# Optimization experiments

Hardware: AMD Instinct MI355X
Metric: run time of the kernel (lower is better)

Reference implementation:

```python
import jax, jax.numpy as jnp
import numpy as np

TOP_K = 2


def setup_inputs() -> dict:
    key = jax.random.key(0)
    k_x, k_w = jax.random.split(key)
    B, S, D, E = 4, 4096, 2048, 64
    x = jax.random.normal(k_x, (B, S, D), dtype=jnp.float32)
    # nn.Linear weight has shape [num_experts, d_model]
    W_r = jax.random.normal(k_w, (E, D), dtype=jnp.float32) * (1.0 / np.sqrt(D))
    return {"x": x, "W_r": W_r}


def reference(x, W_r):
    # router logits: [B, S, E]
    logits = jnp.einsum("bsd,ed->bse", x, W_r)
    router_probs = jax.nn.softmax(logits, axis=-1)
    gate_weights, expert_idx = jax.lax.top_k(router_probs, TOP_K)
    gate_weights = gate_weights / jnp.sum(gate_weights, axis=-1, keepdims=True)
    return gate_weights, expert_idx, router_probs
```

## Files before the change

### kernel.cpp

```cpp
#include <hip/hip_runtime.h>
#include <stdint.h>
#include <math.h>

#define D    2048
#define E    64
#define ROWS 16384
#define RG   64
#define BK   64
#define EW   16

typedef const __attribute__((address_space(1))) unsigned int guint;
typedef __attribute__((address_space(3))) unsigned int luint;
typedef __attribute__((ext_vector_type(16))) float f32x16;

__device__ __forceinline__ void gl_lds16(const float* g, float* l) {
    __builtin_amdgcn_global_load_lds((guint*)g, (luint*)l, 16, 0, 0);
}

template<int NSPLIT>
__global__ __launch_bounds__(256, 4)
void logits_kernel(const float* __restrict__ x, const float* __restrict__ Wr,
                   float* __restrict__ P) {
    __shared__ float XS[2][RG * BK];

    const int tid  = threadIdx.x;
    const int lane = tid & 63;
    const int wu   = __builtin_amdgcn_readfirstlane(tid >> 6);
    const int bid  = blockIdx.x;
    const int ks   = bid % NSPLIT;
    const int rg   = bid / NSPLIT;
    const int row0 = rg * RG;
    const int kbase = ks * (D / NSPLIT);
    const int NCH  = (D / NSPLIT) / BK;

    const float* xg[4];
#pragma unroll
    for (int i = 0; i < 4; ++i) {
        const int row = i * 16 + (tid >> 4);
        const int kq  = ((tid & 15) ^ (row & 7)) * 4;
        xg[i] = x + (size_t)(row0 + row) * D + kbase + kq;
    }
    float* const xsl0 = &XS[0][tid * 4];
    float* const xsl1 = &XS[1][tid * 4];

#define STAGE(buf, kc) do {                                                   \
        _Pragma("unroll")                                                     \
        for (int i = 0; i < 4; ++i)                                           \
            gl_lds16(xg[i] + (kc) * BK, ((buf) ? xsl1 : xsl0) + i * 1024);    \
    } while (0)

    const int eb = wu * EW;
    const float* const wbase = Wr + (size_t)eb * D + kbase;

    float acc[EW];
#pragma unroll
    for (int e = 0; e < EW; ++e) acc[e] = 0.0f;

    STAGE(0, 0);
    __syncthreads();

    const int swf = (lane & 7) * 4;
    int cur = 0;
    for (int c = 0; c < NCH; ++c) {
        if (c + 1 < NCH) STAGE(cur ^ 1, c + 1);

        float4 xv[16];
        const float* xr = &XS[cur][lane * BK];
#pragma unroll
        for (int q = 0; q < 16; ++q)
            xv[q] = *(const float4*)(xr + ((q * 4) ^ swf));

#pragma unroll
        for (int e = 0; e < EW; ++e) {
            const float* wr_ = wbase + (size_t)e * D + c * BK;
#pragma unroll
            for (int g = 0; g < 4; ++g) {
                const f32x16 wv = *(const f32x16*)(wr_ + g * 16);
#pragma unroll
                for (int j = 0; j < 4; ++j) {
                    const float4 xq = xv[g * 4 + j];
                    acc[e] = fmaf(xq.x, wv[j * 4 + 0], acc[e]);
                    acc[e] = fmaf(xq.y, wv[j * 4 + 1], acc[e]);
                    acc[e] = fmaf(xq.z, wv[j * 4 + 2], acc[e]);
                    acc[e] = fmaf(xq.w, wv[j * 4 + 3], acc[e]);
                }
            }
        }
        __syncthreads();
        cur ^= 1;
    }

    float* const pr = P + ((size_t)ks * ROWS + row0 + lane) * E + eb;
#pragma unroll
    for (int e = 0; e < EW; ++e) pr[e] = acc[e];
#undef STAGE
}

template<int NSPLIT>
__global__ __launch_bounds__(256, 8)
void finish_kernel(const float* __restrict__ P, float* __restrict__ out) {
    const int lane = threadIdx.x & 63;
    const int w    = threadIdx.x >> 6;
    const int row  = blockIdx.x * 4 + w;

    float v = 0.0f;
#pragma unroll
    for (int s = 0; s < NSPLIT; ++s)
        v += P[((size_t)s * ROWS + row) * E + lane];

    float* const out_gw    = out;
    float* const out_idx   = out + 32768;
    float* const out_probs = out + 65536;

    float m = v;
#pragma unroll
    for (int off = 32; off; off >>= 1) m = fmaxf(m, __shfl_xor(m, off));
    const float p = __expf(v - m);
    float s = p;
#pragma unroll
    for (int off = 32; off; off >>= 1) s += __shfl_xor(s, off);
    const float inv_s = 1.0f / s;

    out_probs[(size_t)row * 64 + lane] = p * inv_s;

    float v1 = v; int i1 = lane;
#pragma unroll
    for (int off = 32; off; off >>= 1) {
        const float ov = __shfl_xor(v1, off);
        const int   oi = __shfl_xor(i1, off);
        if (ov > v1 || (ov == v1 && oi < i1)) { v1 = ov; i1 = oi; }
    }
    float v2 = (lane == i1) ? -INFINITY : v; int i2 = lane;
#pragma unroll
    for (int off = 32; off; off >>= 1) {
        const float ov = __shfl_xor(v2, off);
        const int   oi = __shfl_xor(i2, off);
        if (ov > v2 || (ov == v2 && oi < i2)) { v2 = ov; i2 = oi; }
    }

    if (lane == 0) {
        const float p1 = __expf(v1 - m) * inv_s;
        const float p2 = __expf(v2 - m) * inv_s;
        const float inv12 = 1.0f / (p1 + p2);
        out_gw[(size_t)row * 2 + 0]  = p1 * inv12;
        out_gw[(size_t)row * 2 + 1]  = p2 * inv12;
        out_idx[(size_t)row * 2 + 0] = (float)i1;
        out_idx[(size_t)row * 2 + 1] = (float)i2;
    }
}

extern "C" void kernel_launch(void* const* d_in, const int* in_sizes, int n_in,
                              void* d_out, int out_size, void* d_ws, size_t ws_size,
                              hipStream_t stream) {
    const float* x  = (const float*)d_in[0];
    const float* Wr = (const float*)d_in[1];
    float* out = (float*)d_out;
    float* P   = (float*)d_ws;

    const size_t need4 = (size_t)4 * ROWS * E * sizeof(float);
    if (ws_size >= need4) {
        hipLaunchKernelGGL((logits_kernel<4>), dim3(256 * 4), dim3(256), 0, stream, x, Wr, P);
        hipLaunchKernelGGL((finish_kernel<4>), dim3(ROWS / 4), dim3(256), 0, stream, P, out);
    } else {
        hipLaunchKernelGGL((logits_kernel<1>), dim3(256), dim3(256), 0, stream, x, Wr, P);
        hipLaunchKernelGGL((finish_kernel<1>), dim3(ROWS / 4), dim3(256), 0, stream, P, out);
    }
}
```

Measured before the change: 112.1 us.

## Enlarge row tile to 256 rows per block with 4 rows per thread

Each block now covers 256 rows instead of 64, and each thread accumulates 4 rows by 16 experts, so every W_r float4 load is reused across 4 rows. This cuts repeated global and L1 reads of the router weights. The grid shrinks to 256 blocks, each using 128KB of LDS at 1 block per CU, and the barrier moves to the start of each chunk after an explicit vmcnt wait. The price is lower occupancy, more register pressure from 64 accumulators, and fewer blocks than CUs available to hide latency.

```diff
diff --git a/kernel.cpp b/kernel.cpp
--- a/kernel.cpp
+++ b/kernel.cpp
@@ -5,23 +5,22 @@
 #define D    2048
 #define E    64
 #define ROWS 16384
-#define RG   64
+#define RB   256
 #define BK   64
 #define EW   16
 
 typedef const __attribute__((address_space(1))) unsigned int guint;
 typedef __attribute__((address_space(3))) unsigned int luint;
-typedef __attribute__((ext_vector_type(16))) float f32x16;
 
 __device__ __forceinline__ void gl_lds16(const float* g, float* l) {
     __builtin_amdgcn_global_load_lds((guint*)g, (luint*)l, 16, 0, 0);
 }
 
 template<int NSPLIT>
-__global__ __launch_bounds__(256, 4)
+__global__ __launch_bounds__(256, 1)
 void logits_kernel(const float* __restrict__ x, const float* __restrict__ Wr,
                    float* __restrict__ P) {
-    __shared__ float XS[2][RG * BK];
+    __shared__ float XS[2][RB * BK];
 
     const int tid  = threadIdx.x;
     const int lane = tid & 63;
@@ -29,70 +28,78 @@
     const int bid  = blockIdx.x;
     const int ks   = bid % NSPLIT;
     const int rg   = bid / NSPLIT;
-    const int row0 = rg * RG;
-    const int kbase = ks * (D / NSPLIT);
+    const int row0 = rg * RB;
+    const int kb   = ks * (D / NSPLIT);
     const int NCH  = (D / NSPLIT) / BK;
 
-    const float* xg[4];
-#pragma unroll
-    for (int i = 0; i < 4; ++i) {
-        const int row = i * 16 + (tid >> 4);
-        const int kq  = ((tid & 15) ^ (row & 7)) * 4;
-        xg[i] = x + (size_t)(row0 + row) * D + kbase + kq;
-    }
-    float* const xsl0 = &XS[0][tid * 4];
-    float* const xsl1 = &XS[1][tid * 4];
+    int vz;
+    asm volatile("v_mov_b32 %0, 0" : "=v"(vz));
 
-#define STAGE(buf, kc) do {                                                   \
+    const float* const xstage =
+        x + (size_t)(row0 + (tid >> 4)) * D + kb + (((tid & 15) ^ (tid >> 4)) << 2);
+
+#define STAGE(b, cc) do {                                                     \
         _Pragma("unroll")                                                     \
-        for (int i = 0; i < 4; ++i)                                           \
-            gl_lds16(xg[i] + (kc) * BK, ((buf) ? xsl1 : xsl0) + i * 1024);    \
+        for (int i = 0; i < 16; ++i)                                          \
+            gl_lds16(xstage + (size_t)(cc) * BK + (size_t)i * 16 * D,         \
+                     &XS[b][i * 1024 + tid * 4]);                             \
     } while (0)
 
     const int eb = wu * EW;
-    const float* const wbase = Wr + (size_t)eb * D + kbase;
+    const float* we[EW];
+#pragma unroll
+    for (int e = 0; e < EW; ++e)
+        we[e] = Wr + (size_t)(eb + e) * D + kb + vz;
 
-    float acc[EW];
+    float acc[4][EW];
 #pragma unroll
-    for (int e = 0; e < EW; ++e) acc[e] = 0.0f;
+    for (int j = 0; j < 4; ++j)
+#pragma unroll
+        for (int e = 0; e < EW; ++e) acc[j][e] = 0.0f;
 
     STAGE(0, 0);
-    __syncthreads();
 
-    const int swf = (lane & 7) * 4;
+    const int swq = (lane & 15) << 2;
     int cur = 0;
     for (int c = 0; c < NCH; ++c) {
+        asm volatile("s_waitcnt vmcnt(0)" ::: "memory");
+        __syncthreads();
         if (c + 1 < NCH) STAGE(cur ^ 1, c + 1);
 
-        float4 xv[16];
-        const float* xr = &XS[cur][lane * BK];
+        const float* const xb = &XS[cur][0];
+        int rowf[4];
 #pragma unroll
-        for (int q = 0; q < 16; ++q)
-            xv[q] = *(const float4*)(xr + ((q * 4) ^ swf));
+        for (int j = 0; j < 4; ++j) rowf[j] = (64 * j + lane) * BK;
 
 #pragma unroll
-        for (int e = 0; e < EW; ++e) {
-            const float* wr_ = wbase + (size_t)e * D + c * BK;
+        for (int kq = 0; kq < 16; ++kq) {
+            float4 xq[4];
 #pragma unroll
-            for (int g = 0; g < 4; ++g) {
-                const f32x16 wv = *(const f32x16*)(wr_ + g * 16);
+            for (int j = 0; j < 4; ++j)
+                xq[j] = *(const float4*)(xb + rowf[j] + (swq ^ (kq << 2)));
+#pragma unroll
+            for (int e = 0; e < EW; ++e) {
+                const float4 wv = *(const float4*)(we[e] + c * BK + kq * 4);
 #pragma unroll
                 for (int j = 0; j < 4; ++j) {
-                    const float4 xq = xv[g * 4 + j];
-                    acc[e] = fmaf(xq.x, wv[j * 4 + 0], acc[e]);
-                    acc[e] = fmaf(xq.y, wv[j * 4 + 1], acc[e]);
-                    acc[e] = fmaf(xq.z, wv[j * 4 + 2], acc[e]);
-                    acc[e] = fmaf(xq.w, wv[j * 4 + 3], acc[e]);
+                    acc[j][e] = fmaf(xq[j].x, wv.x, acc[j][e]);
+                    acc[j][e] = fmaf(xq[j].y, wv.y, acc[j][e]);
+                    acc[j][e] = fmaf(xq[j].z, wv.z, acc[j][e]);
+                    acc[j][e] = fmaf(xq[j].w, wv.w, acc[j][e]);
                 }
             }
         }
-        __syncthreads();
         cur ^= 1;
     }
 
-    float* const pr = P + ((size_t)ks * ROWS + row0 + lane) * E + eb;
 #pragma unroll
-    for (int e = 0; e < EW; ++e) pr[e] = acc[e];
+    for (int j = 0; j < 4; ++j) {
+        float* const pr = P + ((size_t)ks * ROWS + row0 + 64 * j + lane) * E + eb;
+#pragma unroll
+        for (int g = 0; g < 4; ++g)
+            *(float4*)(pr + 4 * g) = make_float4(acc[j][4 * g + 0], acc[j][4 * g + 1],
+                                                 acc[j][4 * g + 2], acc[j][4 * g + 3]);
+    }
 #undef STAGE
 }
 
@@ -159,10 +166,10 @@
 
     const size_t need4 = (size_t)4 * ROWS * E * sizeof(float);
     if (ws_size >= need4) {
-        hipLaunchKernelGGL((logits_kernel<4>), dim3(256 * 4), dim3(256), 0, stream, x, Wr, P);
+        hipLaunchKernelGGL((logits_kernel<4>), dim3((ROWS / RB) * 4), dim3(256), 0, stream, x, Wr, P);
         hipLaunchKernelGGL((finish_kernel<4>), dim3(ROWS / 4), dim3(256), 0, stream, P, out);
     } else {
-        hipLaunchKernelGGL((logits_kernel<1>), dim3(256), dim3(256), 0, stream, x, Wr, P);
+        hipLaunchKernelGGL((logits_kernel<1>), dim3(ROWS / RB), dim3(256), 0, stream, x, Wr, P);
         hipLaunchKernelGGL((finish_kernel<1>), dim3(ROWS / 4), dim3(256), 0, stream, P, out);
     }
 }
```

Result: slower. 120.2 us (+7.2%).
